# Performance work log

Hardware: AMD Instinct MI355X
Metric: run time of the kernel (lower is better)

Reference implementation:

```python
import jax, jax.numpy as jnp
import numpy as np

B, L, D, E, K = 4, 2048, 2048, 8, 2
H = 4 * D  # expert hidden dim


def setup_inputs() -> dict:
    key = jax.random.key(0)
    k0, k1, k2, k3 = jax.random.split(key, 4)
    s = 0.02  # init scale for weights
    x = jax.random.normal(k0, (B, L, D), dtype=jnp.float32)
    gate_w = jax.random.normal(k1, (E, D), dtype=jnp.float32) * s   # Linear(dim, E) weight [out,in]
    w1 = jax.random.normal(k2, (E, H, D), dtype=jnp.float32) * s     # Linear(D, 4D) per expert
    w2 = jax.random.normal(k3, (E, D, H), dtype=jnp.float32) * s     # Linear(4D, D) per expert
    return {"x": x, "gate_w": gate_w, "w1": w1, "w2": w2}


def reference(x, gate_w, w1, w2):
    # Gating: logits [B,L,E], top-k over experts, softmax over the k selected logits
    gate_logits = jnp.einsum('bld,ed->ble', x, gate_w)
    topk_logits, topk_idx = jax.lax.top_k(gate_logits, K)         # [B,L,K]
    gates = jax.nn.softmax(topk_logits, axis=-1)                   # [B,L,K]
    onehot = jax.nn.one_hot(topk_idx, E, dtype=x.dtype)            # [B,L,K,E]
    # Combined per-expert weight: sum_i gate_i * 1[idx_i == e]  -> [B,L,E]
    combine = jnp.einsum('blk,blke->ble', gates, onehot)

    # Dense all-expert FFN (matches the original's math: outputs += mask*gate*expert(x))
    out = jnp.zeros_like(x)
    for e in range(E):  # small fixed expert count
        h = jax.nn.gelu(jnp.einsum('bld,hd->blh', x, w1[e]), approximate=False)
        out = out + combine[..., e:e + 1] * jnp.einsum('blh,dh->bld', h, w2[e])

    # Load-balance loss: expert_counts starts at zero, updated with this batch's one-hot sums
    counts = onehot.sum(axis=(0, 1, 2))                            # [E]
    p = counts / counts.sum()
    loss = jnp.mean((p - 1.0 / E) ** 2)
    return out, loss
```

## Files before the change

### kernel.cpp

```cpp
#include <hip/hip_runtime.h>
#include <hip/hip_bf16.h>
#include <math.h>

#define NTOK 8192
#define DDIM 2048
#define EEXP 8
#define HDIM 8192
#define BM 128
#define BN 128
#define BK 64

typedef __attribute__((ext_vector_type(8))) short short8;
typedef __attribute__((ext_vector_type(4))) float f32x4;
typedef __attribute__((ext_vector_type(4))) unsigned short u16x4;

#define WS_CNT   0
#define WS_BASE  64
#define WS_LIST  1024
#define WS_GATE  (1024 + EEXP*NTOK*4)
#define WS_XB    (1u<<20)
#define WS_H     (WS_XB + (size_t)NTOK*DDIM*2)

__device__ __forceinline__ unsigned short f2bf(float f) {
  union { float f; unsigned int u; } v; v.f = f;
  unsigned int r = v.u + 0x7fffu + ((v.u >> 16) & 1u);
  return (unsigned short)(r >> 16);
}

#define GLD_LDS16(g, l)                                                        \
  __builtin_amdgcn_global_load_lds((__attribute__((address_space(1))) void*)(g), \
                                   (__attribute__((address_space(3))) void*)(l), \
                                   16, 0, 0)

__global__ __launch_bounds__(256) void gate_kernel(
    const float* __restrict__ x, const float* __restrict__ gw,
    unsigned short* __restrict__ xb, int* __restrict__ cnt,
    int* __restrict__ list, float* __restrict__ gatev)
{
  __shared__ float red[EEXP][256];
  const int tid = threadIdx.x;
  const int t = blockIdx.x;
  const float* xr = x + (size_t)t * DDIM;
  float acc[EEXP];
#pragma unroll
  for (int e = 0; e < EEXP; ++e) acc[e] = 0.f;
  for (int d = tid; d < DDIM; d += 256) {
    float xv = xr[d];
    xb[(size_t)t * DDIM + d] = f2bf(xv);
#pragma unroll
    for (int e = 0; e < EEXP; ++e) acc[e] += xv * gw[e * DDIM + d];
  }
#pragma unroll
  for (int e = 0; e < EEXP; ++e) red[e][tid] = acc[e];
  __syncthreads();
  for (int s = 128; s > 0; s >>= 1) {
    if (tid < s) {
#pragma unroll
      for (int e = 0; e < EEXP; ++e) red[e][tid] += red[e][tid + s];
    }
    __syncthreads();
  }
  if (tid == 0) {
    float l[EEXP];
#pragma unroll
    for (int e = 0; e < EEXP; ++e) l[e] = red[e][0];
    int i0 = 0;
#pragma unroll
    for (int e = 1; e < EEXP; ++e) if (l[e] > l[i0]) i0 = e;
    int i1 = (i0 == 0) ? 1 : 0;
#pragma unroll
    for (int e = 0; e < EEXP; ++e) { if (e != i0 && l[e] > l[i1]) i1 = e; }
    float ex = expf(l[i1] - l[i0]);
    float g0 = 1.f / (1.f + ex);
    float g1 = ex / (1.f + ex);
    int p0 = atomicAdd(&cnt[i0], 1);
    list[i0 * NTOK + p0] = t; gatev[i0 * NTOK + p0] = g0;
    int p1 = atomicAdd(&cnt[i1], 1);
    list[i1 * NTOK + p1] = t; gatev[i1 * NTOK + p1] = g1;
  }
}

__global__ void prefix_loss_kernel(const int* __restrict__ cnt,
                                   int* __restrict__ base,
                                   float* __restrict__ loss_out)
{
  if (threadIdx.x == 0 && blockIdx.x == 0) {
    int b = 0;
    for (int e = 0; e < EEXP; ++e) { base[e] = b; b += cnt[e]; }
    base[EEXP] = b;
    float tot = (float)b;
    float loss = 0.f;
    for (int e = 0; e < EEXP; ++e) {
      float p = (float)cnt[e] / tot - 0.125f;
      loss += p * p;
    }
    *loss_out = loss * 0.125f;
  }
}

__global__ __launch_bounds__(256) void gemm1_kernel(
    const unsigned short* __restrict__ xb, const float* __restrict__ w1,
    unsigned short* __restrict__ hbuf,
    const int* __restrict__ cnt, const int* __restrict__ base,
    const int* __restrict__ list)
{
  __shared__ unsigned short sA[BM * BK];
  __shared__ unsigned short sB[BN * BK];
  __shared__ int sTok[BM];

  const int e = blockIdx.y >> 6;
  const int tilem = blockIdx.y & 63;
  const int Me = cnt[e];
  if (tilem * BM >= Me) return;
  const int cb = blockIdx.x * BN;
  const int tid = threadIdx.x;
  const int lane = tid & 63;
  const int wave = tid >> 6;

  if (tid < BM) {
    int pos = tilem * BM + tid;
    sTok[tid] = list[e * NTOK + min(pos, Me - 1)];
  }
  __syncthreads();

  const float* w1e = w1 + (size_t)e * HDIM * DDIM;

  const int acol = (tid & 7) * 8;
  const unsigned short* aptr[4];
#pragma unroll
  for (int s = 0; s < 4; ++s) {
    int r = (tid >> 3) + 32 * s;
    aptr[s] = xb + (size_t)sTok[r] * DDIM + acol;
  }
  const int k4 = tid & 15;
  const int n0 = tid >> 4;
  const float* bptr[8];
  int boff[8];
#pragma unroll
  for (int i2 = 0; i2 < 8; ++i2) {
    int n = n0 + 16 * i2;
    bptr[i2] = w1e + (size_t)(cb + n) * DDIM + k4 * 4;
    boff[i2] = n * BK + k4 * 4;
  }

  f32x4 acc[4][4];
  const f32x4 zero = {0.f, 0.f, 0.f, 0.f};
#pragma unroll
  for (int i = 0; i < 4; ++i)
#pragma unroll
    for (int j = 0; j < 4; ++j) acc[i][j] = zero;

  const int wm = (wave & 1) * 64;
  const int wn = (wave >> 1) * 64;
  const int quad = lane >> 4;
  const int l16 = lane & 15;

  for (int k0 = 0; k0 < DDIM; k0 += BK) {
    f32x4 bv[8];
#pragma unroll
    for (int i2 = 0; i2 < 8; ++i2)
      bv[i2] = *(const f32x4*)(bptr[i2] + k0);
#pragma unroll
    for (int s = 0; s < 4; ++s)
      GLD_LDS16(aptr[s] + k0, sA + wave * 512 + s * 2048);
#pragma unroll
    for (int i2 = 0; i2 < 8; ++i2) {
      u16x4 pk;
      pk[0] = f2bf(bv[i2][0]); pk[1] = f2bf(bv[i2][1]);
      pk[2] = f2bf(bv[i2][2]); pk[3] = f2bf(bv[i2][3]);
      *(u16x4*)(sB + boff[i2]) = pk;
    }
    __syncthreads();
#pragma unroll
    for (int kk = 0; kk < BK; kk += 32) {
      short8 af[4], bf[4];
#pragma unroll
      for (int i = 0; i < 4; ++i)
        af[i] = *(const short8*)(sA + (wm + i * 16 + l16) * BK + kk + quad * 8);
#pragma unroll
      for (int j = 0; j < 4; ++j)
        bf[j] = *(const short8*)(sB + (wn + j * 16 + l16) * BK + kk + quad * 8);
#pragma unroll
      for (int i = 0; i < 4; ++i)
#pragma unroll
        for (int j = 0; j < 4; ++j)
          acc[i][j] = __builtin_amdgcn_mfma_f32_16x16x32_bf16(af[i], bf[j], acc[i][j], 0, 0, 0);
    }
    __syncthreads();
  }

  const int pb = base[e];
#pragma unroll
  for (int i = 0; i < 4; ++i) {
#pragma unroll
    for (int r = 0; r < 4; ++r) {
      int rowl = wm + i * 16 + quad * 4 + r;
      int pos = tilem * BM + rowl;
      if (pos < Me) {
        size_t hrow = (size_t)(pb + pos) * HDIM + cb + wn;
#pragma unroll
        for (int j = 0; j < 4; ++j) {
          float v = acc[i][j][r];
          float g = 0.5f * v * (1.f + erff(v * 0.70710678118654752440f));
          hbuf[hrow + j * 16 + l16] = f2bf(g);
        }
      }
    }
  }
}

__global__ __launch_bounds__(256) void gemm2_kernel(
    const unsigned short* __restrict__ hbuf, const float* __restrict__ w2,
    float* __restrict__ out,
    const int* __restrict__ cnt, const int* __restrict__ base,
    const int* __restrict__ list, const float* __restrict__ gatev)
{
  __shared__ unsigned short sA[BM * BK];
  __shared__ unsigned short sB[BN * BK];
  __shared__ int sTok[BM];
  __shared__ float sGate[BM];

  const int e = blockIdx.y >> 6;
  const int tilem = blockIdx.y & 63;
  const int Me = cnt[e];
  if (tilem * BM >= Me) return;
  const int cb = blockIdx.x * BN;
  const int tid = threadIdx.x;
  const int lane = tid & 63;
  const int wave = tid >> 6;
  const int pb = base[e];

  if (tid < BM) {
    int pos = tilem * BM + tid;
    int posc = min(pos, Me - 1);
    sTok[tid] = list[e * NTOK + posc];
    sGate[tid] = gatev[e * NTOK + posc];
  }
  __syncthreads();

  const float* w2e = w2 + (size_t)e * DDIM * HDIM;

  const int acol = (tid & 7) * 8;
  const unsigned short* aptr[4];
#pragma unroll
  for (int s = 0; s < 4; ++s) {
    int pos = tilem * BM + (tid >> 3) + 32 * s;
    aptr[s] = hbuf + (size_t)(pb + min(pos, Me - 1)) * HDIM + acol;
  }
  const int k4 = tid & 15;
  const int n0 = tid >> 4;
  const float* bptr[8];
  int boff[8];
#pragma unroll
  for (int i2 = 0; i2 < 8; ++i2) {
    int n = n0 + 16 * i2;
    bptr[i2] = w2e + (size_t)(cb + n) * HDIM + k4 * 4;
    boff[i2] = n * BK + k4 * 4;
  }

  f32x4 acc[4][4];
  const f32x4 zero = {0.f, 0.f, 0.f, 0.f};
#pragma unroll
  for (int i = 0; i < 4; ++i)
#pragma unroll
    for (int j = 0; j < 4; ++j) acc[i][j] = zero;

  const int wm = (wave & 1) * 64;
  const int wn = (wave >> 1) * 64;
  const int quad = lane >> 4;
  const int l16 = lane & 15;

  for (int k0 = 0; k0 < HDIM; k0 += BK) {
    f32x4 bv[8];
#pragma unroll
    for (int i2 = 0; i2 < 8; ++i2)
      bv[i2] = *(const f32x4*)(bptr[i2] + k0);
#pragma unroll
    for (int s = 0; s < 4; ++s)
      GLD_LDS16(aptr[s] + k0, sA + wave * 512 + s * 2048);
#pragma unroll
    for (int i2 = 0; i2 < 8; ++i2) {
      u16x4 pk;
      pk[0] = f2bf(bv[i2][0]); pk[1] = f2bf(bv[i2][1]);
      pk[2] = f2bf(bv[i2][2]); pk[3] = f2bf(bv[i2][3]);
      *(u16x4*)(sB + boff[i2]) = pk;
    }
    __syncthreads();
#pragma unroll
    for (int kk = 0; kk < BK; kk += 32) {
      short8 af[4], bf[4];
#pragma unroll
      for (int i = 0; i < 4; ++i)
        af[i] = *(const short8*)(sA + (wm + i * 16 + l16) * BK + kk + quad * 8);
#pragma unroll
      for (int j = 0; j < 4; ++j)
        bf[j] = *(const short8*)(sB + (wn + j * 16 + l16) * BK + kk + quad * 8);
#pragma unroll
      for (int i = 0; i < 4; ++i)
#pragma unroll
        for (int j = 0; j < 4; ++j)
          acc[i][j] = __builtin_amdgcn_mfma_f32_16x16x32_bf16(af[i], bf[j], acc[i][j], 0, 0, 0);
    }
    __syncthreads();
  }

#pragma unroll
  for (int i = 0; i < 4; ++i) {
#pragma unroll
    for (int r = 0; r < 4; ++r) {
      int rowl = wm + i * 16 + quad * 4 + r;
      int pos = tilem * BM + rowl;
      if (pos < Me) {
        int tok = sTok[rowl];
        float gt = sGate[rowl];
        float* orow = out + (size_t)tok * DDIM + cb + wn;
#pragma unroll
        for (int j = 0; j < 4; ++j)
          unsafeAtomicAdd(orow + j * 16 + l16, gt * acc[i][j][r]);
      }
    }
  }
}

extern "C" void kernel_launch(void* const* d_in, const int* in_sizes, int n_in,
                              void* d_out, int out_size, void* d_ws, size_t ws_size,
                              hipStream_t stream)
{
  const float* x  = (const float*)d_in[0];
  const float* gw = (const float*)d_in[1];
  const float* w1 = (const float*)d_in[2];
  const float* w2 = (const float*)d_in[3];
  float* out = (float*)d_out;
  char* ws = (char*)d_ws;

  int*   cnt   = (int*)(ws + WS_CNT);
  int*   base  = (int*)(ws + WS_BASE);
  int*   list  = (int*)(ws + WS_LIST);
  float* gatev = (float*)(ws + WS_GATE);
  unsigned short* xb = (unsigned short*)(ws + WS_XB);
  unsigned short* hb = (unsigned short*)(ws + WS_H);

  hipMemsetAsync(d_out, 0, (size_t)out_size * sizeof(float), stream);
  hipMemsetAsync(ws, 0, 1024, stream);

  gate_kernel<<<NTOK, 256, 0, stream>>>(x, gw, xb, cnt, list, gatev);
  prefix_loss_kernel<<<1, 64, 0, stream>>>(cnt, base, out + (size_t)NTOK * DDIM);
  gemm1_kernel<<<dim3(HDIM / BN, 512), 256, 0, stream>>>(xb, w1, hb, cnt, base, list);
  gemm2_kernel<<<dim3(DDIM / BN, 512), 256, 0, stream>>>(hb, w2, out, cnt, base, list, gatev);
}
```

Baseline: 3.555 ms.

## Swizzle LDS tiles, use packed bf16 convert, vectorize gate kernel loads

Result: faster. 3.230 ms (-9.1%).

```diff
diff --git a/kernel.cpp b/kernel.cpp
--- a/kernel.cpp
+++ b/kernel.cpp
@@ -12,7 +12,7 @@
 
 typedef __attribute__((ext_vector_type(8))) short short8;
 typedef __attribute__((ext_vector_type(4))) float f32x4;
-typedef __attribute__((ext_vector_type(4))) unsigned short u16x4;
+typedef __attribute__((ext_vector_type(2))) unsigned int u32x2;
 
 #define WS_CNT   0
 #define WS_BASE  64
@@ -27,6 +27,12 @@
   return (unsigned short)(r >> 16);
 }
 
+__device__ __forceinline__ unsigned int cvt_pk_bf16(float lo, float hi) {
+  unsigned int r;
+  asm("v_cvt_pk_bf16_f32 %0, %1, %2" : "=v"(r) : "v"(lo), "v"(hi));
+  return r;
+}
+
 #define GLD_LDS16(g, l)                                                        \
   __builtin_amdgcn_global_load_lds((__attribute__((address_space(1))) void*)(g), \
                                    (__attribute__((address_space(3))) void*)(l), \
@@ -40,15 +46,24 @@
   __shared__ float red[EEXP][256];
   const int tid = threadIdx.x;
   const int t = blockIdx.x;
-  const float* xr = x + (size_t)t * DDIM;
+  const float4* xr4 = (const float4*)(x + (size_t)t * DDIM);
+  const float4* gw4 = (const float4*)gw;
   float acc[EEXP];
 #pragma unroll
   for (int e = 0; e < EEXP; ++e) acc[e] = 0.f;
-  for (int d = tid; d < DDIM; d += 256) {
-    float xv = xr[d];
-    xb[(size_t)t * DDIM + d] = f2bf(xv);
-#pragma unroll
-    for (int e = 0; e < EEXP; ++e) acc[e] += xv * gw[e * DDIM + d];
+#pragma unroll
+  for (int it = 0; it < DDIM / 4 / 256; ++it) {
+    int d4 = tid + it * 256;
+    float4 xv = xr4[d4];
+    u32x2 pk;
+    pk[0] = cvt_pk_bf16(xv.x, xv.y);
+    pk[1] = cvt_pk_bf16(xv.z, xv.w);
+    *(u32x2*)(xb + (size_t)t * DDIM + d4 * 4) = pk;
+#pragma unroll
+    for (int e = 0; e < EEXP; ++e) {
+      float4 g = gw4[e * (DDIM / 4) + d4];
+      acc[e] += xv.x * g.x + xv.y * g.y + xv.z * g.z + xv.w * g.w;
+    }
   }
 #pragma unroll
   for (int e = 0; e < EEXP; ++e) red[e][tid] = acc[e];
@@ -125,7 +140,7 @@
 
   const float* w1e = w1 + (size_t)e * HDIM * DDIM;
 
-  const int acol = (tid & 7) * 8;
+  const int acol = (((tid & 7) ^ ((tid >> 3) & 7)) * 8);
   const unsigned short* aptr[4];
 #pragma unroll
   for (int s = 0; s < 4; ++s) {
@@ -134,13 +149,14 @@
   }
   const int k4 = tid & 15;
   const int n0 = tid >> 4;
+  const int bswz = (n0 & 7) << 4;
   const float* bptr[8];
-  int boff[8];
+  int boffb[8];
 #pragma unroll
   for (int i2 = 0; i2 < 8; ++i2) {
     int n = n0 + 16 * i2;
     bptr[i2] = w1e + (size_t)(cb + n) * DDIM + k4 * 4;
-    boff[i2] = n * BK + k4 * 4;
+    boffb[i2] = n * 128 + ((k4 * 8) ^ bswz);
   }
 
   f32x4 acc[4][4];
@@ -154,6 +170,16 @@
   const int wn = (wave >> 1) * 64;
   const int quad = lane >> 4;
   const int l16 = lane & 15;
+  const int rswz = (l16 & 7) << 4;
+  int aRow[4], bRow[4];
+#pragma unroll
+  for (int i = 0; i < 4; ++i) aRow[i] = (wm + i * 16 + l16) * 128;
+#pragma unroll
+  for (int j = 0; j < 4; ++j) bRow[j] = (wn + j * 16 + l16) * 128;
+  const int col0 = (quad * 16) ^ rswz;
+  const int col1 = (64 + quad * 16) ^ rswz;
+  const char* sAc = (const char*)sA;
+  const char* sBc = (const char*)sB;
 
   for (int k0 = 0; k0 < DDIM; k0 += BK) {
     f32x4 bv[8];
@@ -165,21 +191,22 @@
       GLD_LDS16(aptr[s] + k0, sA + wave * 512 + s * 2048);
 #pragma unroll
     for (int i2 = 0; i2 < 8; ++i2) {
-      u16x4 pk;
-      pk[0] = f2bf(bv[i2][0]); pk[1] = f2bf(bv[i2][1]);
-      pk[2] = f2bf(bv[i2][2]); pk[3] = f2bf(bv[i2][3]);
-      *(u16x4*)(sB + boff[i2]) = pk;
-    }
-    __syncthreads();
-#pragma unroll
-    for (int kk = 0; kk < BK; kk += 32) {
+      u32x2 pk;
+      pk[0] = cvt_pk_bf16(bv[i2][0], bv[i2][1]);
+      pk[1] = cvt_pk_bf16(bv[i2][2], bv[i2][3]);
+      *(u32x2*)((char*)sB + boffb[i2]) = pk;
+    }
+    __syncthreads();
+#pragma unroll
+    for (int kki = 0; kki < 2; ++kki) {
+      const int colb = kki ? col1 : col0;
       short8 af[4], bf[4];
 #pragma unroll
       for (int i = 0; i < 4; ++i)
-        af[i] = *(const short8*)(sA + (wm + i * 16 + l16) * BK + kk + quad * 8);
+        af[i] = *(const short8*)(sAc + aRow[i] + colb);
 #pragma unroll
       for (int j = 0; j < 4; ++j)
-        bf[j] = *(const short8*)(sB + (wn + j * 16 + l16) * BK + kk + quad * 8);
+        bf[j] = *(const short8*)(sBc + bRow[j] + colb);
 #pragma unroll
       for (int i = 0; i < 4; ++i)
 #pragma unroll
@@ -240,7 +267,7 @@
 
   const float* w2e = w2 + (size_t)e * DDIM * HDIM;
 
-  const int acol = (tid & 7) * 8;
+  const int acol = (((tid & 7) ^ ((tid >> 3) & 7)) * 8);
   const unsigned short* aptr[4];
 #pragma unroll
   for (int s = 0; s < 4; ++s) {
@@ -249,13 +276,14 @@
   }
   const int k4 = tid & 15;
   const int n0 = tid >> 4;
+  const int bswz = (n0 & 7) << 4;
   const float* bptr[8];
-  int boff[8];
+  int boffb[8];
 #pragma unroll
   for (int i2 = 0; i2 < 8; ++i2) {
     int n = n0 + 16 * i2;
     bptr[i2] = w2e + (size_t)(cb + n) * HDIM + k4 * 4;
-    boff[i2] = n * BK + k4 * 4;
+    boffb[i2] = n * 128 + ((k4 * 8) ^ bswz);
   }
 
   f32x4 acc[4][4];
@@ -269,6 +297,16 @@
   const int wn = (wave >> 1) * 64;
   const int quad = lane >> 4;
   const int l16 = lane & 15;
+  const int rswz = (l16 & 7) << 4;
+  int aRow[4], bRow[4];
+#pragma unroll
+  for (int i = 0; i < 4; ++i) aRow[i] = (wm + i * 16 + l16) * 128;
+#pragma unroll
+  for (int j = 0; j < 4; ++j) bRow[j] = (wn + j * 16 + l16) * 128;
+  const int col0 = (quad * 16) ^ rswz;
+  const int col1 = (64 + quad * 16) ^ rswz;
+  const char* sAc = (const char*)sA;
+  const char* sBc = (const char*)sB;
 
   for (int k0 = 0; k0 < HDIM; k0 += BK) {
     f32x4 bv[8];
@@ -280,21 +318,22 @@
       GLD_LDS16(aptr[s] + k0, sA + wave * 512 + s * 2048);
 #pragma unroll
     for (int i2 = 0; i2 < 8; ++i2) {
-      u16x4 pk;
-      pk[0] = f2bf(bv[i2][0]); pk[1] = f2bf(bv[i2][1]);
-      pk[2] = f2bf(bv[i2][2]); pk[3] = f2bf(bv[i2][3]);
-      *(u16x4*)(sB + boff[i2]) = pk;
-    }
-    __syncthreads();
-#pragma unroll
-    for (int kk = 0; kk < BK; kk += 32) {
+      u32x2 pk;
+      pk[0] = cvt_pk_bf16(bv[i2][0], bv[i2][1]);
+      pk[1] = cvt_pk_bf16(bv[i2][2], bv[i2][3]);
+      *(u32x2*)((char*)sB + boffb[i2]) = pk;
+    }
+    __syncthreads();
+#pragma unroll
+    for (int kki = 0; kki < 2; ++kki) {
+      const int colb = kki ? col1 : col0;
       short8 af[4], bf[4];
 #pragma unroll
       for (int i = 0; i < 4; ++i)
-        af[i] = *(const short8*)(sA + (wm + i * 16 + l16) * BK + kk + quad * 8);
+        af[i] = *(const short8*)(sAc + aRow[i] + colb);
 #pragma unroll
       for (int j = 0; j < 4; ++j)
-        bf[j] = *(const short8*)(sB + (wn + j * 16 + l16) * BK + kk + quad * 8);
+        bf[j] = *(const short8*)(sBc + bRow[j] + colb);
 #pragma unroll
       for (int i = 0; i < 4; ++i)
 #pragma unroll
```
